# Optimization experiments

Hardware: AMD Instinct MI355X
Metric: run time of the kernel (lower is better)

The kernel has to match this reference:

```python
import jax, jax.numpy as jnp
import numpy as np

B, T, NE = 8, 256, 64
H = 512
NH = 4
NTOKS = 32000
VOCAB = 32000


def setup_inputs() -> dict:
    key = jax.random.key(0)
    ks = jax.random.split(key, 20)
    s = 0.02
    return {
        "outp": jax.random.randint(ks[0], (B, T), 0, NTOKS),
        "ents": jax.random.normal(ks[1], (B, NE, H), jnp.float32),
        "entlens": jax.random.randint(ks[2], (B,), 1, NE),
        "emb": jax.random.normal(ks[3], (NTOKS, H), jnp.float32) * s,
        "W_ih": jax.random.normal(ks[4], (4 * H, 2 * H), jnp.float32) * s,
        "W_hh": jax.random.normal(ks[5], (4 * H, H), jnp.float32) * s,
        "b_ih": jnp.zeros((4 * H,), jnp.float32),
        "b_hh": jnp.zeros((4 * H,), jnp.float32),
        "Wq": jax.random.normal(ks[6], (H, H), jnp.float32) * s,
        "Wk": jax.random.normal(ks[7], (H, H), jnp.float32) * s,
        "Wv": jax.random.normal(ks[8], (H, H), jnp.float32) * s,
        "out_W": jax.random.normal(ks[9], (VOCAB, 2 * H), jnp.float32) * s,
        "out_b": jnp.zeros((VOCAB,), jnp.float32),
        "sw_W": jax.random.normal(ks[10], (1, 2 * H), jnp.float32) * s,
        "sw_b": jnp.zeros((1,), jnp.float32),
        "mattn_W": jax.random.normal(ks[11], (H, 2 * H), jnp.float32) * s,
        "mattn_b": jnp.zeros((H,), jnp.float32),
    }


def reference(outp, ents, entlens, emb, W_ih, W_hh, b_ih, b_hh, Wq, Wk, Wv,
              out_W, out_b, sw_W, sw_b, mattn_W, mattn_b):
    b, ne, h = ents.shape
    hd = h // NH
    # maskFromList: valid where arange(ne) <= entlens; True = masked out
    invalid = jnp.arange(ne)[None, :] > entlens[:, None]  # [B, NE]
    neg = jnp.float32(-1e30)

    hx0 = ents.mean(axis=1)  # glob init (non-graph path)
    cx0 = hx0
    # precompute K, V per head (keys = ents)
    K = (ents @ Wk.T).reshape(b, ne, NH, hd)
    V = (ents @ Wv.T).reshape(b, ne, NH, hd)
    scale = 1.0 / jnp.sqrt(jnp.float32(h))  # GraphWriter scales by sqrt(full key_dim)

    def mha(hx):
        q = (hx @ Wq.T).reshape(b, NH, hd)
        att = jnp.einsum('bhd,bnhd->bhn', q, K) * scale
        att = jnp.where(invalid[:, None, :], neg, att)
        att = jax.nn.softmax(att, axis=-1)
        return jnp.einsum('bhn,bnhd->bhd', att, V).reshape(b, h)

    e_t = jnp.swapaxes(emb[outp], 0, 1)  # [T, B, H]

    def step(carry, k):
        hx, cx, a = carry
        prev = jnp.concatenate([a, k], axis=1)  # [B, 2H]
        gates = prev @ W_ih.T + b_ih + hx @ W_hh.T + b_hh
        i, f, g, o = jnp.split(gates, 4, axis=1)
        cx = jax.nn.sigmoid(f) * cx + jax.nn.sigmoid(i) * jnp.tanh(g)
        hx = jax.nn.sigmoid(o) * jnp.tanh(cx)
        a = mha(hx)
        return (hx, cx, a), jnp.concatenate([hx, a], axis=1)

    _, outs = jax.lax.scan(step, (hx0, cx0, jnp.zeros_like(hx0)), e_t)
    l = jnp.swapaxes(outs, 0, 1)  # [B, T, 2H]

    s = jax.nn.sigmoid(l @ sw_W.T + sw_b)                     # [B, T, 1]
    o = jax.nn.softmax(l @ out_W.T + out_b, axis=2) * s       # [B, T, V]
    # MatrixAttn pointer distribution over entities
    dec = l @ mattn_W.T + mattn_b                             # [B, T, H]
    unnorm = jnp.einsum('bth,bnh->btn', dec, ents)
    unnorm = jnp.where(invalid[:, None, :], neg, unnorm)
    z = jax.nn.softmax(unnorm, axis=2) * (1.0 - s)            # [B, T, NE]
    full = jnp.concatenate([o, z], axis=2) + 1e-6
    return jnp.log(full), z
```

## Files before the change

### kernel.cpp

```cpp
#include <hip/hip_runtime.h>
#include <cstdint>

#define TT 256
#define BB 8
#define NE 64
#define HH 512
#define VOCAB 32000
#define G4 2048
#define RS 32064
#define MROWS 2048
#define SCALE 0.044194173824159216f

typedef _Float16 h2 __attribute__((ext_vector_type(2)));
typedef _Float16 h8 __attribute__((ext_vector_type(8)));
typedef float f4 __attribute__((ext_vector_type(4)));
typedef unsigned long long u64;

__device__ inline float sigf(float x){ return 1.f/(1.f+__expf(-x)); }

__device__ inline u64 g64load(const u64* p){
  return __hip_atomic_load((u64*)p, __ATOMIC_RELAXED, __HIP_MEMORY_SCOPE_AGENT);
}
__device__ inline void g64store(u64* p, u64 v){
  __hip_atomic_store(p, v, __ATOMIC_RELAXED, __HIP_MEMORY_SCOPE_AGENT);
}

__global__ __launch_bounds__(256) void cast_k(const float* __restrict__ src, _Float16* __restrict__ dst,
    int total, int src_ld, int src_off, int dst_ld, int dst_off, int cshift, int lo, float mul, int tr)
{
  int i = blockIdx.x*256 + threadIdx.x;
  if (i >= total) return;
  int c = i & ((1<<cshift)-1);
  int r = i >> cshift;
  float x = src[(long)r*src_ld + src_off + c] * mul;
  _Float16 h = (_Float16)x;
  if (lo) h = (_Float16)(x - (float)h);
  if (tr) dst[(long)c*dst_ld + dst_off + r] = h;
  else    dst[(long)r*dst_ld + dst_off + c] = h;
}

__global__ __launch_bounds__(256) void embgather_k(const float* __restrict__ emb,
    const int* __restrict__ outp, _Float16* __restrict__ dst)
{
  int i = blockIdx.x*256 + threadIdx.x;
  int k = i & 511; int m = i >> 9;
  int t = m >> 3, b = m & 7;
  int tok = outp[b*TT + t];
  dst[i] = (_Float16)emb[(long)tok*HH + k];
}

__global__ __launch_bounds__(256) void prep_k(const float* __restrict__ b_ih, const float* __restrict__ b_hh,
    const float* __restrict__ ents, float* bsum, u64* hxe, u64* Se)
{
  int i = blockIdx.x*256 + threadIdx.x;
  if (i < G4) bsum[i] = b_ih[i] + b_hh[i];
  if (i < BB*HH) {
    int b = i >> 9, j = i & 511;
    float s = 0.f;
    for (int n = 0; n < NE; n++) s += ents[(size_t)((b<<6)+n)*HH + j];
    s *= (1.0f/NE);
    hxe[i] = (u64)__float_as_uint(s);
  }
  if (i < BB*256) Se[i] = 0ull;
}

__global__ __launch_bounds__(256) void vblk_k(const float* __restrict__ Vb,
    _Float16* __restrict__ VblkS, _Float16* __restrict__ VblkT)
{
  int i = blockIdx.x*256 + threadIdx.x;
  int he = i & 255, d = (i >> 8) & 511, b = i >> 17;
  _Float16 v = (_Float16)0.f;
  if ((he >> 6) == (d >> 7)) v = (_Float16)Vb[(((long)((b<<6)|(he&63)))<<9) + d];
  VblkT[(((long)((b<<9)|d))<<8) + he] = v;
  VblkS[(((long)((b<<8)|he))<<9) + d] = v;
}

__global__ __launch_bounds__(256) void gemm_k(const _Float16* __restrict__ A, const _Float16* __restrict__ Bm,
    float* __restrict__ C, const float* __restrict__ bias,
    int M, int N, int K, int lda, int ldb, int ldc, int accum, long sA, long sB, long sC)
{
  __shared__ __align__(16) _Float16 At[128][40];
  __shared__ __align__(16) _Float16 Bt[128][40];
  int z = blockIdx.z;
  A  += (long)z * sA;  Bm += (long)z * sB;  C += (long)z * sC;
  int tid = threadIdx.x;
  int n0 = blockIdx.x * 128, m0 = blockIdx.y * 128;
  int wave = tid >> 6, lane = tid & 63;
  int mw = (wave & 1) << 6, nw = (wave >> 1) << 6;
  int lr = tid >> 2, lc = (tid & 3) << 3;
  const _Float16* Ap0 = A + (long)(m0 + lr)*lda + lc;
  const _Float16* Ap1 = Ap0 + (long)64*lda;
  const _Float16* Bp0 = Bm + (long)(n0 + lr)*ldb + lc;
  const _Float16* Bp1 = Bp0 + (long)64*ldb;
  f4 acc[4][4] = {};
  int rr = lane & 15, kq = (lane >> 4) << 3;
  for (int kt = 0; kt < K; kt += 32) {
    h8 av0 = *(const h8*)(Ap0 + kt);
    h8 av1 = *(const h8*)(Ap1 + kt);
    h8 bv0 = *(const h8*)(Bp0 + kt);
    h8 bv1 = *(const h8*)(Bp1 + kt);
    __syncthreads();
    *(h8*)&At[lr][lc]    = av0;
    *(h8*)&At[64+lr][lc] = av1;
    *(h8*)&Bt[lr][lc]    = bv0;
    *(h8*)&Bt[64+lr][lc] = bv1;
    __syncthreads();
    h8 af[4], bf[4];
    #pragma unroll
    for (int mt=0;mt<4;mt++) af[mt] = *(const h8*)&At[mw + mt*16 + rr][kq];
    #pragma unroll
    for (int nt=0;nt<4;nt++) bf[nt] = *(const h8*)&Bt[nw + nt*16 + rr][kq];
    #pragma unroll
    for (int mt=0;mt<4;mt++)
      #pragma unroll
      for (int nt=0;nt<4;nt++)
        acc[mt][nt] = __builtin_amdgcn_mfma_f32_16x16x32_f16(af[mt], bf[nt], acc[mt][nt], 0, 0, 0);
  }
  int cc = lane & 15, rq = (lane >> 4) << 2;
  #pragma unroll
  for (int nt=0;nt<4;nt++) {
    int col = n0 + nw + nt*16 + cc;
    float bv = bias ? bias[col] : 0.f;
    #pragma unroll
    for (int mt=0;mt<4;mt++) {
      int row0 = m0 + mw + mt*16 + rq;
      #pragma unroll
      for (int r=0;r<4;r++) {
        long idx = (long)(row0 + r)*ldc + col;
        float v = acc[mt][nt][r] + bv;
        if (accum) C[idx] += v; else C[idx] = v;
      }
    }
  }
}

__global__ __launch_bounds__(512, 1) void rnn_k(
    const float* __restrict__ gates_pre, const _Float16* __restrict__ Whh16,
    const float* __restrict__ Mh, const float* __restrict__ WVall,
    const int* __restrict__ entlens,
    u64* hxe, u64* Se, _Float16* Pg, _Float16* l_h, _Float16* l_lo)
{
  __shared__ __align__(16) _Float16 Wl[64][528];
  __shared__ __align__(16) float    Ml[8][516];
  __shared__ __align__(16) _Float16 WVl[64][264];
  __shared__ __align__(16) float    hxs[512];
  __shared__ __align__(16) _Float16 hxh[512];
  __shared__ __align__(16) _Float16 ph[256];
  __shared__ float gsum[64];
  __shared__ float gpl[64];

  const int tid = threadIdx.x, wg = blockIdx.x;
  const int b = wg >> 5, wgl = wg & 31, u_off = wgl << 4;
  const int lane = tid & 63, wv = tid >> 6;
  const int el = entlens[b];
  const int h_own = wgl >> 3, e_base = (wgl & 7) << 3;
  u64* hxb = hxe + ((long)b << 9);
  u64* Sb  = Se  + ((long)b << 8);

  for (int i = tid; i < 64*64; i += 512) {
    int r = i >> 6, c8 = (i & 63) << 3;
    int grow = ((r >> 4) << 9) + u_off + (r & 15);
    *(h8*)&Wl[r][c8] = *(const h8*)(Whh16 + ((long)grow << 9) + c8);
  }
  for (int i = tid; i < 8*128; i += 512) {
    int r = i >> 7, c4 = (i & 127) << 2;
    const float* src = Mh + ((long)h_own << 18) + (((long)((b << 6) + e_base + r)) << 9) + c4;
    *(f4*)&Ml[r][c4] = *(const f4*)src;
  }
  for (int i = tid; i < 64*256; i += 512) {
    int r = i >> 8, c = i & 255;
    int grow = ((r >> 4) << 9) + u_off + (r & 15);
    WVl[r][c] = (_Float16)WVall[((long)grow << 11) + (b << 8) + c];
  }
  if (tid < 256) {
    u64 w0 = g64load(hxb + 2*tid), w1 = g64load(hxb + 2*tid + 1);
    float f0 = __uint_as_float((unsigned)w0), f1 = __uint_as_float((unsigned)w1);
    hxs[2*tid] = f0; hxs[2*tid+1] = f1;
    hxh[2*tid] = (_Float16)f0; hxh[2*tid+1] = (_Float16)f1;
  }
  __syncthreads();
  float cx = 0.f;
  if (wv == 0 && lane < 16) cx = hxs[u_off + lane];

  for (int it = 0; it < TT; it++) {
    const unsigned set = (unsigned)(it + 1);
    {
      float sp = 0.f;
      const float* mr = &Ml[wv][lane << 3];
      const float* hp = &hxs[lane << 3];
      #pragma unroll
      for (int j = 0; j < 8; j++) sp += hp[j] * mr[j];
      #pragma unroll
      for (int off = 32; off; off >>= 1) sp += __shfl_xor(sp, off);
      if (lane == 0)
        g64store(Sb + (h_own << 6) + e_base + wv,
                 ((u64)set << 32) | (u64)__float_as_uint(sp));
    }
    if (tid < 64) {
      int col = ((tid >> 4) << 9) + u_off + (tid & 15);
      gpl[tid] = gates_pre[((long)((it << 3) + b) << 11) + col];
    }
    {
      int r = tid >> 3, sl = tid & 7;
      float s = 0.f;
      #pragma unroll
      for (int c = 0; c < 8; c++) {
        int k = (sl << 6) + (c << 3);
        union { h8 v; h2 p[4]; } a_, w_;
        a_.v = *(const h8*)&hxh[k];
        w_.v = *(const h8*)&Wl[r][k];
        #pragma unroll
        for (int p = 0; p < 4; p++) s = __builtin_amdgcn_fdot2(a_.p[p], w_.p[p], s, false);
      }
      s += __shfl_xor(s, 1); s += __shfl_xor(s, 2); s += __shfl_xor(s, 4);
      if (sl == 0) gsum[r] = s;
    }
    __syncthreads();
    if (wv == 0) {
      u64 sv[4];
      #pragma unroll
      for (int j = 0; j < 4; j++) sv[j] = g64load(Sb + (j << 6) + lane);
      for (;;) {
        bool ok = true;
        #pragma unroll
        for (int j = 0; j < 4; j++) if ((unsigned)(sv[j] >> 32) < set) ok = false;
        if (ok) break;
        __builtin_amdgcn_s_sleep(1);
        #pragma unroll
        for (int j = 0; j < 4; j++)
          if ((unsigned)(sv[j] >> 32) < set) sv[j] = g64load(Sb + (j << 6) + lane);
      }
      float wvp = 0.f;
      if (it > 0) {
        #pragma unroll
        for (int j = 0; j < 4; j++) {
          float x = __uint_as_float((unsigned)sv[j]);
          if (lane > el) x = -1e30f;
          float mx = x;
          #pragma unroll
          for (int off = 32; off; off >>= 1) mx = fmaxf(mx, __shfl_xor(mx, off));
          float e = __expf(x - mx), sm = e;
          #pragma unroll
          for (int off = 32; off; off >>= 1) sm += __shfl_xor(sm, off);
          float p = e / sm;
          _Float16 p16 = (_Float16)p;
          ph[(j << 6) + lane] = p16;
          Pg[((long)((b << 8) + (it - 1)) << 8) + (j << 6) + lane] = p16;
        }
        float s = 0.f;
        #pragma unroll
        for (int c = 0; c < 32; c++) {
          union { h8 v; h2 p[4]; } pv, wv_;
          pv.v  = *(const h8*)&ph[c << 3];
          wv_.v = *(const h8*)&WVl[lane][c << 3];
          #pragma unroll
          for (int p2 = 0; p2 < 4; p2++) s = __builtin_amdgcn_fdot2(pv.p[p2], wv_.p[p2], s, false);
        }
        wvp = s;
      }
      float gv = gpl[lane] + gsum[lane] + wvp;
      float gi = __shfl(gv, lane & 15);
      float gf = __shfl(gv, 16 + (lane & 15));
      float gg = __shfl(gv, 32 + (lane & 15));
      float go = __shfl(gv, 48 + (lane & 15));
      if (lane < 16) {
        float c_ = sigf(gf)*cx + sigf(gi)*tanhf(gg);
        cx = c_;
        float h = sigf(go)*tanhf(c_);
        int j = u_off + lane;
        g64store(hxb + j, ((u64)set << 32) | (u64)__float_as_uint(h));
        _Float16 hh_ = (_Float16)h;
        long li = ((long)((b << 8) + it)) << 10;
        l_h[li + j]  = hh_;
        l_lo[li + j] = (_Float16)(h - (float)hh_);
      }
    }
    if (tid < 256) {
      u64 w0 = g64load(hxb + 2*tid), w1 = g64load(hxb + 2*tid + 1);
      while ((unsigned)(w0 >> 32) < set) { __builtin_amdgcn_s_sleep(1); w0 = g64load(hxb + 2*tid); }
      while ((unsigned)(w1 >> 32) < set) { __builtin_amdgcn_s_sleep(1); w1 = g64load(hxb + 2*tid + 1); }
      float f0 = __uint_as_float((unsigned)w0), f1 = __uint_as_float((unsigned)w1);
      hxs[2*tid] = f0; hxs[2*tid+1] = f1;
      hxh[2*tid] = (_Float16)f0; hxh[2*tid+1] = (_Float16)f1;
    }
    __syncthreads();
  }
  {
    float sp = 0.f;
    const float* mr = &Ml[wv][lane << 3];
    const float* hp = &hxs[lane << 3];
    #pragma unroll
    for (int j = 0; j < 8; j++) sp += hp[j] * mr[j];
    #pragma unroll
    for (int off = 32; off; off >>= 1) sp += __shfl_xor(sp, off);
    if (lane == 0)
      g64store(Sb + (h_own << 6) + e_base + wv, ((u64)257u << 32) | (u64)__float_as_uint(sp));
    if (wv == 0) {
      u64 sv[4];
      #pragma unroll
      for (int j = 0; j < 4; j++) sv[j] = g64load(Sb + (j << 6) + lane);
      for (;;) {
        bool ok = true;
        #pragma unroll
        for (int j = 0; j < 4; j++) if ((unsigned)(sv[j] >> 32) < 257u) ok = false;
        if (ok) break;
        __builtin_amdgcn_s_sleep(1);
        #pragma unroll
        for (int j = 0; j < 4; j++)
          if ((unsigned)(sv[j] >> 32) < 257u) sv[j] = g64load(Sb + (j << 6) + lane);
      }
      #pragma unroll
      for (int j = 0; j < 4; j++) {
        float x = __uint_as_float((unsigned)sv[j]);
        if (lane > el) x = -1e30f;
        float mx = x;
        #pragma unroll
        for (int off = 32; off; off >>= 1) mx = fmaxf(mx, __shfl_xor(mx, off));
        float e = __expf(x - mx), sm = e;
        #pragma unroll
        for (int off = 32; off; off >>= 1) sm += __shfl_xor(sm, off);
        Pg[((long)((b << 8) + 255) << 8) + (j << 6) + lane] = (_Float16)(e / sm);
      }
    }
  }
}

__global__ __launch_bounds__(256) void stats_k(const float* __restrict__ out0,
    const _Float16* __restrict__ l_h, const float* __restrict__ swW, const float* __restrict__ swb,
    float* rowmax, float* rowsum, float* sgate)
{
  int m = blockIdx.x, tid = threadIdx.x;
  const float* row = out0 + (long)m*RS;
  float mx = -1e30f, sm = 0.f;
  for (int c = tid; c < VOCAB; c += 256) {
    float x = row[c];
    float nm = fmaxf(mx, x);
    sm = sm*__expf(mx-nm) + __expf(x-nm);
    mx = nm;
  }
  float sd = 0.f;
  const _Float16* lr_ = l_h + ((long)m << 10);
  for (int k = tid; k < 1024; k += 256) sd += (float)lr_[k] * swW[k];
  #pragma unroll
  for (int off=32; off>0; off>>=1) {
    float omx = __shfl_xor(mx, off), osm = __shfl_xor(sm, off);
    float nm = fmaxf(mx, omx);
    sm = sm*__expf(mx-nm) + osm*__expf(omx-nm);
    mx = nm;
    sd += __shfl_xor(sd, off);
  }
  __shared__ float smx[4], ssm[4], ssd[4];
  int wv = tid >> 6;
  if ((tid & 63) == 0) { smx[wv]=mx; ssm[wv]=sm; ssd[wv]=sd; }
  __syncthreads();
  if (tid == 0) {
    float M = smx[0], S = ssm[0], D = ssd[0];
    for (int w2=1;w2<4;w2++) {
      float nm = fmaxf(M, smx[w2]);
      S = S*__expf(M-nm) + ssm[w2]*__expf(smx[w2]-nm);
      M = nm; D += ssd[w2];
    }
    rowmax[m] = M; rowsum[m] = S;
    sgate[m] = 1.f/(1.f + __expf(-(D + swb[0])));
  }
}

__global__ __launch_bounds__(256) void fin_k(float* __restrict__ out,
    const float* __restrict__ dec, const float* __restrict__ ents, const int* __restrict__ entlens,
    const float* __restrict__ rowmax, const float* __restrict__ rowsum, const float* __restrict__ sgate)
{
  int m = blockIdx.x, tid = threadIdx.x;
  int b = m >> 8;
  __shared__ float dl[512];
  for (int i = tid; i < 512; i += 256) dl[i] = dec[((long)m<<9) + i];
  __syncthreads();
  float s = sgate[m];
  if (tid < 64) {
    int n = tid;
    const float* ep = ents + (((long)((b<<6)+n)) << 9);
    float uq = 0.f;
    for (int k=0;k<512;k+=4)
      uq += dl[k]*ep[k] + dl[k+1]*ep[k+1] + dl[k+2]*ep[k+2] + dl[k+3]*ep[k+3];
    if (n > entlens[b]) uq = -1e30f;
    float mx = uq;
    #pragma unroll
    for (int off=32; off>0; off>>=1) mx = fmaxf(mx, __shfl_xor(mx, off));
    float e = __expf(uq - mx);
    float sum = e;
    #pragma unroll
    for (int off=32; off>0; off>>=1) sum += __shfl_xor(sum, off);
    float z = (e/sum) * (1.f - s);
    out[(long)m*RS + VOCAB + n] = __logf(z + 1e-6f);
    out[(long)MROWS*RS + ((long)m<<6) + n] = z;
  }
  float mx = rowmax[m], inv = 1.f/rowsum[m];
  for (int c = tid; c < VOCAB; c += 256) {
    long idx = (long)m*RS + c;
    float x = out[idx];
    out[idx] = __logf(__expf(x - mx)*inv*s + 1e-6f);
  }
}

extern "C" void kernel_launch(void* const* d_in, const int* in_sizes, int n_in,
                              void* d_out, int out_size, void* d_ws, size_t ws_size,
                              hipStream_t stream)
{
  const int*   outp    = (const int*)d_in[0];
  const float* ents    = (const float*)d_in[1];
  const int*   entlens = (const int*)d_in[2];
  const float* emb     = (const float*)d_in[3];
  const float* W_ih    = (const float*)d_in[4];
  const float* W_hh    = (const float*)d_in[5];
  const float* b_ih    = (const float*)d_in[6];
  const float* b_hh    = (const float*)d_in[7];
  const float* Wq      = (const float*)d_in[8];
  const float* Wk      = (const float*)d_in[9];
  const float* Wv      = (const float*)d_in[10];
  const float* out_W   = (const float*)d_in[11];
  const float* out_b   = (const float*)d_in[12];
  const float* sw_W    = (const float*)d_in[13];
  const float* sw_b    = (const float*)d_in[14];
  const float* mattn_W = (const float*)d_in[15];
  const float* mattn_b = (const float*)d_in[16];
  float* out = (float*)d_out;
  (void)in_sizes; (void)n_in; (void)out_size; (void)ws_size;

  char* w = (char*)d_ws;
  size_t off = 0;
  auto alloc = [&](size_t bytes) -> char* {
    char* p = w + off; off += bytes; off = (off + 255) & ~(size_t)255; return p;
  };
  _Float16* outW_h = (_Float16*)alloc((size_t)VOCAB*1024*2);
  _Float16* l_h    = (_Float16*)alloc((size_t)MROWS*1024*2);
  _Float16* l_lo   = (_Float16*)alloc((size_t)MROWS*1024*2);
  float*    gpre   = (float*)alloc((size_t)MROWS*2048*4);
  _Float16* Wihk_h = (_Float16*)alloc((size_t)2048*512*2);
  _Float16* Wiha16 = (_Float16*)alloc((size_t)2048*512*2);
  _Float16* Whh16  = (_Float16*)alloc((size_t)2048*512*2);
  _Float16* emb_h  = (_Float16*)alloc((size_t)2048*512*2);
  _Float16* ents_h = (_Float16*)alloc((size_t)512*512*2);
  _Float16* Wk_h   = (_Float16*)alloc((size_t)512*512*2);
  _Float16* Wv_h   = (_Float16*)alloc((size_t)512*512*2);
  _Float16* WqT16  = (_Float16*)alloc((size_t)512*512*2);
  _Float16* mat_h  = (_Float16*)alloc((size_t)512*1024*2);
  _Float16* mat_lo = (_Float16*)alloc((size_t)512*1024*2);
  float*    Kb     = (float*)alloc((size_t)512*512*4);
  float*    Vb     = (float*)alloc((size_t)512*512*4);
  _Float16* Kb16   = (_Float16*)alloc((size_t)512*512*2);
  float*    Mh     = (float*)alloc((size_t)4*512*512*4);
  _Float16* VblkS  = (_Float16*)alloc((size_t)2048*512*2);
  _Float16* VblkT  = (_Float16*)alloc((size_t)8*512*256*2);
  float*    WVall  = (float*)alloc((size_t)2048*2048*4);
  _Float16* Pg     = (_Float16*)alloc((size_t)8*256*256*2);
  float*    dec    = (float*)alloc((size_t)MROWS*512*4);
  float*    bsum   = (float*)alloc(2048*4);
  u64*      hxe    = (u64*)alloc((size_t)4096*8);
  u64*      Se     = (u64*)alloc((size_t)2048*8);
  float*    rmax   = (float*)alloc(2048*4);
  float*    rsum   = (float*)alloc(2048*4);
  float*    sg     = (float*)alloc(2048*4);
  float*    Af     = gpre;

  auto cast = [&](const float* s, _Float16* d, int total, int sld, int soff, int dld, int doff,
                  int cs, int lo, float mul, int tr) {
    cast_k<<<(total+255)/256, 256, 0, stream>>>(s, d, total, sld, soff, dld, doff, cs, lo, mul, tr);
  };
  auto gemm = [&](const _Float16* A, const _Float16* B, float* C, const float* bias,
                  int M, int N, int K, int lda, int ldb, int ldc, int accum,
                  int gx, int gy, int gz, long sA, long sB, long sC) {
    gemm_k<<<dim3(gx,gy,gz), 256, 0, stream>>>(A, B, C, bias, M, N, K, lda, ldb, ldc, accum, sA, sB, sC);
  };

  cast(out_W,   outW_h, VOCAB*1024, 1024, 0,   1024, 0,   10, 0, 1.f, 0);
  cast(W_ih,    Wihk_h, 2048*512,   1024, 512, 512,  0,   9,  0, 1.f, 0);
  cast(W_ih,    Wiha16, 2048*512,   1024, 0,   512,  0,   9,  0, 1.f, 0);
  cast(W_hh,    Whh16,  2048*512,   512,  0,   512,  0,   9,  0, 1.f, 0);
  cast(Wq,      WqT16,  512*512,    512,  0,   512,  0,   9,  0, 1.f, 1);
  cast(Wk,      Wk_h,   512*512,    512,  0,   512,  0,   9,  0, 1.f, 0);
  cast(Wv,      Wv_h,   512*512,    512,  0,   512,  0,   9,  0, 1.f, 0);
  cast(mattn_W, mat_h,  512*1024,   1024, 0,   1024, 0,   10, 0, 1.f, 0);
  cast(mattn_W, mat_lo, 512*1024,   1024, 0,   1024, 0,   10, 1, 1.f, 0);
  cast(ents,    ents_h, 512*512,    512,  0,   512,  0,   9,  0, 1.f, 0);

  embgather_k<<<4096, 256, 0, stream>>>(emb, outp, emb_h);
  prep_k<<<16, 256, 0, stream>>>(b_ih, b_hh, ents, bsum, hxe, Se);

  gemm(ents_h, Wk_h,   Kb,   nullptr, 512,  512,  512, 512, 512, 512,  0,  4,  4, 1, 0,0,0);
  gemm(ents_h, Wv_h,   Vb,   nullptr, 512,  512,  512, 512, 512, 512,  0,  4,  4, 1, 0,0,0);
  gemm(emb_h,  Wihk_h, gpre, bsum,    2048, 2048, 512, 512, 512, 2048, 0, 16, 16, 1, 0,0,0);

  cast(Kb, Kb16, 512*512, 512, 0, 512, 0, 9, 0, SCALE, 0);
  vblk_k<<<4096, 256, 0, stream>>>(Vb, VblkS, VblkT);

  for (int h = 0; h < 4; h++)
    gemm(Kb16 + h*128, WqT16 + h*128, Mh + (long)h*512*512, nullptr,
         512, 512, 128, 512, 512, 512, 0, 4, 4, 1, 0,0,0);
  gemm(Wiha16, VblkS, WVall, nullptr,
       2048, 2048, 512, 512, 512, 2048, 0, 16, 16, 1, 0,0,0);

  rnn_k<<<256, 512, 0, stream>>>(gpre, Whh16, Mh, WVall, entlens, hxe, Se, Pg, l_h, l_lo);

  gemm(Pg, VblkT, Af, nullptr, 256, 512, 256, 256, 256, 512, 0,
       4, 2, 8, (long)256*256, (long)512*256, (long)256*512);
  cast(Af, l_h,  MROWS*512, 512, 0, 1024, 512, 9, 0, 1.f, 0);
  cast(Af, l_lo, MROWS*512, 512, 0, 1024, 512, 9, 1, 1.f, 0);

  gemm(l_h,  mat_h,  dec, mattn_b, 2048, 512,   1024, 1024, 1024, 512, 0, 4,  16, 1, 0,0,0);
  gemm(l_lo, mat_h,  dec, nullptr, 2048, 512,   1024, 1024, 1024, 512, 1, 4,  16, 1, 0,0,0);
  gemm(l_h,  mat_lo, dec, nullptr, 2048, 512,   1024, 1024, 1024, 512, 1, 4,  16, 1, 0,0,0);
  gemm(l_h,  outW_h, out, out_b,   2048, 32000, 1024, 1024, 1024, RS,  0, 250, 16, 1, 0,0,0);

  stats_k<<<2048, 256, 0, stream>>>(out, l_h, sw_W, sw_b, rmax, rsum, sg);
  fin_k<<<2048, 256, 0, stream>>>(out, dec, ents, entlens, rmax, rsum, sg);
}
```

Before: 2.212 ms.

## Split per-head attention softmax across four waves and swizzle LDS weight layouts

The recurrent kernel's attention step, which computed four head softmaxes and the WV dot products serially in one wave, now gives one head to each of four waves. Partial sums are combined through shared memory after a barrier, shortening the serial critical path of each timestep. The Whh, WV and M tiles in LDS are also re-laid out so consecutive lanes read consecutive addresses, which is meant to avoid bank conflicts, and the earlier padding is dropped. In exchange, the barrier now sits after the spin-wait on the attention scores, so every wave waits on the cross-block dependency.

Result: faster. 2.032 ms (-8.1%).

```diff
diff --git a/kernel.cpp b/kernel.cpp
--- a/kernel.cpp
+++ b/kernel.cpp
@@ -140,12 +140,13 @@
     const int* __restrict__ entlens,
     u64* hxe, u64* Se, _Float16* Pg, _Float16* l_h, _Float16* l_lo)
 {
-  __shared__ __align__(16) _Float16 Wl[64][528];
-  __shared__ __align__(16) float    Ml[8][516];
-  __shared__ __align__(16) _Float16 WVl[64][264];
+  __shared__ __align__(16) _Float16 Wl2[32768];
+  __shared__ __align__(16) _Float16 WVl2[16384];
+  __shared__ __align__(16) float    Ml2[8][512];
   __shared__ __align__(16) float    hxs[512];
   __shared__ __align__(16) _Float16 hxh[512];
   __shared__ __align__(16) _Float16 ph[256];
+  __shared__ float part[4][64];
   __shared__ float gsum[64];
   __shared__ float gpl[64];
 
@@ -157,20 +158,21 @@
   u64* hxb = hxe + ((long)b << 9);
   u64* Sb  = Se  + ((long)b << 8);
 
-  for (int i = tid; i < 64*64; i += 512) {
-    int r = i >> 6, c8 = (i & 63) << 3;
+  for (int i = tid; i < 4096; i += 512) {
+    int r = i >> 6, k8c = i & 63;
+    int c = k8c >> 3, sl = k8c & 7;
     int grow = ((r >> 4) << 9) + u_off + (r & 15);
-    *(h8*)&Wl[r][c8] = *(const h8*)(Whh16 + ((long)grow << 9) + c8);
-  }
-  for (int i = tid; i < 8*128; i += 512) {
-    int r = i >> 7, c4 = (i & 127) << 2;
-    const float* src = Mh + ((long)h_own << 18) + (((long)((b << 6) + e_base + r)) << 9) + c4;
-    *(f4*)&Ml[r][c4] = *(const f4*)src;
-  }
-  for (int i = tid; i < 64*256; i += 512) {
-    int r = i >> 8, c = i & 255;
+    *(h8*)&Wl2[((((c << 6) + r) << 3) + sl) << 3] =
+        *(const h8*)(Whh16 + ((long)grow << 9) + (k8c << 3));
+  }
+  for (int i = tid; i < 4096; i += 512) {
+    int r = i >> 9, e = i & 511;
+    Ml2[r][e] = Mh[((long)h_own << 18) + (((long)((b << 6) + e_base + r)) << 9) + e];
+  }
+  for (int i = tid; i < 16384; i += 512) {
+    int r = i >> 8, cj = i & 255, c = cj >> 3, j = cj & 7;
     int grow = ((r >> 4) << 9) + u_off + (r & 15);
-    WVl[r][c] = (_Float16)WVall[((long)grow << 11) + (b << 8) + c];
+    WVl2[((((c << 6) + r) << 3) + j)] = (_Float16)WVall[((long)grow << 11) + (b << 8) + cj];
   }
   if (tid < 256) {
     u64 w0 = g64load(hxb + 2*tid), w1 = g64load(hxb + 2*tid + 1);
@@ -186,78 +188,63 @@
     const unsigned set = (unsigned)(it + 1);
     {
       float sp = 0.f;
-      const float* mr = &Ml[wv][lane << 3];
-      const float* hp = &hxs[lane << 3];
-      #pragma unroll
-      for (int j = 0; j < 8; j++) sp += hp[j] * mr[j];
+      #pragma unroll
+      for (int j = 0; j < 8; j++) sp += hxs[(j << 6) + lane] * Ml2[wv][(j << 6) + lane];
       #pragma unroll
       for (int off = 32; off; off >>= 1) sp += __shfl_xor(sp, off);
       if (lane == 0)
-        g64store(Sb + (h_own << 6) + e_base + wv,
-                 ((u64)set << 32) | (u64)__float_as_uint(sp));
+        g64store(Sb + (h_own << 6) + e_base + wv, ((u64)set << 32) | (u64)__float_as_uint(sp));
     }
     if (tid < 64) {
       int col = ((tid >> 4) << 9) + u_off + (tid & 15);
       gpl[tid] = gates_pre[((long)((it << 3) + b) << 11) + col];
     }
     {
-      int r = tid >> 3, sl = tid & 7;
+      int sl = tid & 7;
       float s = 0.f;
       #pragma unroll
       for (int c = 0; c < 8; c++) {
-        int k = (sl << 6) + (c << 3);
         union { h8 v; h2 p[4]; } a_, w_;
-        a_.v = *(const h8*)&hxh[k];
-        w_.v = *(const h8*)&Wl[r][k];
+        a_.v = *(const h8*)&hxh[(c << 6) + (sl << 3)];
+        w_.v = *(const h8*)&Wl2[((c << 9) + tid) << 3];
         #pragma unroll
         for (int p = 0; p < 4; p++) s = __builtin_amdgcn_fdot2(a_.p[p], w_.p[p], s, false);
       }
       s += __shfl_xor(s, 1); s += __shfl_xor(s, 2); s += __shfl_xor(s, 4);
-      if (sl == 0) gsum[r] = s;
-    }
-    __syncthreads();
-    if (wv == 0) {
-      u64 sv[4];
-      #pragma unroll
-      for (int j = 0; j < 4; j++) sv[j] = g64load(Sb + (j << 6) + lane);
-      for (;;) {
-        bool ok = true;
+      if (sl == 0) gsum[tid >> 3] = s;
+    }
+    if (wv < 4) {
+      u64 sv = g64load(Sb + (wv << 6) + lane);
+      while ((unsigned)(sv >> 32) < set) { __builtin_amdgcn_s_sleep(1); sv = g64load(Sb + (wv << 6) + lane); }
+      if (it > 0) {
+        float x = __uint_as_float((unsigned)sv);
+        if (lane > el) x = -1e30f;
+        float mx = x;
         #pragma unroll
-        for (int j = 0; j < 4; j++) if ((unsigned)(sv[j] >> 32) < set) ok = false;
-        if (ok) break;
-        __builtin_amdgcn_s_sleep(1);
+        for (int off = 32; off; off >>= 1) mx = fmaxf(mx, __shfl_xor(mx, off));
+        float e = __expf(x - mx), sm = e;
         #pragma unroll
-        for (int j = 0; j < 4; j++)
-          if ((unsigned)(sv[j] >> 32) < set) sv[j] = g64load(Sb + (j << 6) + lane);
-      }
-      float wvp = 0.f;
-      if (it > 0) {
-        #pragma unroll
-        for (int j = 0; j < 4; j++) {
-          float x = __uint_as_float((unsigned)sv[j]);
-          if (lane > el) x = -1e30f;
-          float mx = x;
-          #pragma unroll
-          for (int off = 32; off; off >>= 1) mx = fmaxf(mx, __shfl_xor(mx, off));
-          float e = __expf(x - mx), sm = e;
-          #pragma unroll
-          for (int off = 32; off; off >>= 1) sm += __shfl_xor(sm, off);
-          float p = e / sm;
-          _Float16 p16 = (_Float16)p;
-          ph[(j << 6) + lane] = p16;
-          Pg[((long)((b << 8) + (it - 1)) << 8) + (j << 6) + lane] = p16;
-        }
+        for (int off = 32; off; off >>= 1) sm += __shfl_xor(sm, off);
+        float p = e / sm;
+        _Float16 p16 = (_Float16)p;
+        ph[(wv << 6) + lane] = p16;
         float s = 0.f;
         #pragma unroll
-        for (int c = 0; c < 32; c++) {
+        for (int cc = 0; cc < 8; cc++) {
+          int c = (wv << 3) + cc;
           union { h8 v; h2 p[4]; } pv, wv_;
-          pv.v  = *(const h8*)&ph[c << 3];
-          wv_.v = *(const h8*)&WVl[lane][c << 3];
+          pv.v  = *(const h8*)&ph[(wv << 6) + (cc << 3)];
+          wv_.v = *(const h8*)&WVl2[(((c << 6) + lane) << 3)];
           #pragma unroll
           for (int p2 = 0; p2 < 4; p2++) s = __builtin_amdgcn_fdot2(pv.p[p2], wv_.p[p2], s, false);
         }
-        wvp = s;
+        part[wv][lane] = s;
+        Pg[((long)((b << 8) + (it - 1)) << 8) + (wv << 6) + lane] = p16;
       }
+    }
+    __syncthreads();
+    if (wv == 0) {
+      float wvp = (it > 0) ? (part[0][lane] + part[1][lane] + part[2][lane] + part[3][lane]) : 0.f;
       float gv = gpl[lane] + gsum[lane] + wvp;
       float gi = __shfl(gv, lane & 15);
       float gf = __shfl(gv, 16 + (lane & 15));
@@ -287,40 +274,24 @@
   }
   {
     float sp = 0.f;
-    const float* mr = &Ml[wv][lane << 3];
-    const float* hp = &hxs[lane << 3];
-    #pragma unroll
-    for (int j = 0; j < 8; j++) sp += hp[j] * mr[j];
+    #pragma unroll
+    for (int j = 0; j < 8; j++) sp += hxs[(j << 6) + lane] * Ml2[wv][(j << 6) + lane];
     #pragma unroll
     for (int off = 32; off; off >>= 1) sp += __shfl_xor(sp, off);
     if (lane == 0)
       g64store(Sb + (h_own << 6) + e_base + wv, ((u64)257u << 32) | (u64)__float_as_uint(sp));
-    if (wv == 0) {
-      u64 sv[4];
-      #pragma unroll
-      for (int j = 0; j < 4; j++) sv[j] = g64load(Sb + (j << 6) + lane);
-      for (;;) {
-        bool ok = true;
-        #pragma unroll
-        for (int j = 0; j < 4; j++) if ((unsigned)(sv[j] >> 32) < 257u) ok = false;
-        if (ok) break;
-        __builtin_amdgcn_s_sleep(1);
-        #pragma unroll
-        for (int j = 0; j < 4; j++)
-          if ((unsigned)(sv[j] >> 32) < 257u) sv[j] = g64load(Sb + (j << 6) + lane);
-      }
-      #pragma unroll
-      for (int j = 0; j < 4; j++) {
-        float x = __uint_as_float((unsigned)sv[j]);
-        if (lane > el) x = -1e30f;
-        float mx = x;
-        #pragma unroll
-        for (int off = 32; off; off >>= 1) mx = fmaxf(mx, __shfl_xor(mx, off));
-        float e = __expf(x - mx), sm = e;
-        #pragma unroll
-        for (int off = 32; off; off >>= 1) sm += __shfl_xor(sm, off);
-        Pg[((long)((b << 8) + 255) << 8) + (j << 6) + lane] = (_Float16)(e / sm);
-      }
+    if (wv < 4) {
+      u64 sv = g64load(Sb + (wv << 6) + lane);
+      while ((unsigned)(sv >> 32) < 257u) { __builtin_amdgcn_s_sleep(1); sv = g64load(Sb + (wv << 6) + lane); }
+      float x = __uint_as_float((unsigned)sv);
+      if (lane > el) x = -1e30f;
+      float mx = x;
+      #pragma unroll
+      for (int off = 32; off; off >>= 1) mx = fmaxf(mx, __shfl_xor(mx, off));
+      float e = __expf(x - mx), sm = e;
+      #pragma unroll
+      for (int off = 32; off; off >>= 1) sm += __shfl_xor(sm, off);
+      Pg[((long)((b << 8) + 255) << 8) + (wv << 6) + lane] = (_Float16)(e / sm);
     }
   }
 }
```
